# Performance work log

Hardware: AMD Instinct MI355X
Metric: run time of the kernel (lower is better)

## Reference

```python
import jax, jax.numpy as jnp
import numpy as np

N = 512          # number of ROI boxes
C = 1024         # detector box_head feature dim (in_feats)
HID_REPN = 256   # RePN hidden
HID = 256        # GAT hidden per head
HEADS = 4
NUM_CLASSES = 91
IMG_H, IMG_W = 800.0, 800.0
NEG_SLOPE = 0.2  # PyG GATConv default leaky relu slope


def setup_inputs() -> dict:
    key = jax.random.key(0)
    ks = jax.random.split(key, 12)
    s = 0.05
    feats = jax.random.normal(ks[0], (N, C), jnp.float32)
    # valid boxes: x1<x2, y1<y2, inside 800x800 image
    xy = jax.random.uniform(ks[1], (N, 2), jnp.float32, 0.0, 600.0)
    wh = jax.random.uniform(ks[2], (N, 2), jnp.float32, 10.0, 200.0)
    boxes = jnp.concatenate([xy, xy + wh], axis=1)
    # RelationProposalNetwork params (fc1: [hid, 2C+4], fc2: [1, hid])
    repn_w1 = jax.random.normal(ks[3], (HID_REPN, 2 * C + 4), jnp.float32) * s
    repn_b1 = jnp.zeros((HID_REPN,), jnp.float32)
    repn_w2 = jax.random.normal(ks[4], (1, HID_REPN), jnp.float32) * s
    repn_b2 = jnp.zeros((1,), jnp.float32)
    # AttentionalGCN: GATConv1 (in=C+4 -> HID, HEADS, concat), GATConv2 (HEADS*HID -> NUM_CLASSES, 1 head)
    gat1_w = jax.random.normal(ks[5], (C + 4, HEADS * HID), jnp.float32) * s
    gat1_asrc = jax.random.normal(ks[6], (HEADS, HID), jnp.float32) * s
    gat1_adst = jax.random.normal(ks[7], (HEADS, HID), jnp.float32) * s
    gat1_b = jnp.zeros((HEADS * HID,), jnp.float32)
    gat2_w = jax.random.normal(ks[8], (HEADS * HID, NUM_CLASSES), jnp.float32) * s
    gat2_asrc = jax.random.normal(ks[9], (1, NUM_CLASSES), jnp.float32) * s
    gat2_adst = jax.random.normal(ks[10], (1, NUM_CLASSES), jnp.float32) * s
    gat2_b = jnp.zeros((NUM_CLASSES,), jnp.float32)
    return dict(feats=feats, boxes=boxes,
                repn_w1=repn_w1, repn_b1=repn_b1, repn_w2=repn_w2, repn_b2=repn_b2,
                gat1_w=gat1_w, gat1_asrc=gat1_asrc, gat1_adst=gat1_adst, gat1_b=gat1_b,
                gat2_w=gat2_w, gat2_asrc=gat2_asrc, gat2_adst=gat2_adst, gat2_b=gat2_b,
                k=5)


def _gat_conv(x, src, dst, W, a_src, a_dst, bias, n, heads, out_c, concat_heads):
    # PyG GATConv: h = xW, e_uv = leakyrelu(a_src.h_u + a_dst.h_v), softmax over incoming
    # edges of target v, out_v = sum_u alpha_uv h_u (+ bias). Self-loops already in src/dst.
    h = (x @ W).reshape(n, heads, out_c)                       # [N,H,F]
    a_s = jnp.einsum('nhf,hf->nh', h, a_src)                   # [N,H]
    a_d = jnp.einsum('nhf,hf->nh', h, a_dst)
    e = jax.nn.leaky_relu(a_s[src] + a_d[dst], NEG_SLOPE)      # [E,H]
    m = jax.ops.segment_max(e, dst, num_segments=n)            # [N,H]
    m = jnp.where(jnp.isfinite(m), m, 0.0)
    ex = jnp.exp(e - m[dst])
    denom = jax.ops.segment_sum(ex, dst, num_segments=n)
    alpha = ex / (denom[dst] + 1e-16)                          # [E,H]
    out = jax.ops.segment_sum(alpha[:, :, None] * h[src], dst, num_segments=n)  # [N,H,F]
    out = out.reshape(n, heads * out_c) if concat_heads else out.mean(axis=1)
    return out + bias


def reference(feats, boxes, repn_w1, repn_b1, repn_w2, repn_b2,
              gat1_w, gat1_asrc, gat1_adst, gat1_b,
              gat2_w, gat2_asrc, gat2_adst, gat2_b, k):
    n, c = feats.shape
    # --- RelationProposalNetwork: fc1(cat[f_i, f_j, |b_i-b_j|]) without materializing [N,N,2C+4]
    wf1, wf2, wg = repn_w1[:, :c], repn_w1[:, c:2 * c], repn_w1[:, 2 * c:]
    p1 = feats @ wf1.T                                          # [N,hid]
    p2 = feats @ wf2.T                                          # [N,hid]
    geom_pair = jnp.abs(boxes[:, None, :] - boxes[None, :, :])  # [N,N,4]
    pg = jnp.einsum('ijd,hd->ijh', geom_pair, wg)               # [N,N,hid]
    h = jax.nn.relu(p1[:, None, :] + p2[None, :, :] + pg + repn_b1)
    rel = jnp.einsum('ijh,h->ij', h, repn_w2[0]) + repn_b2[0]   # [N,N] relation scores
    # --- kNN graph via topk (skip self at rank 0), as in _make_edge_index (N > k branch)
    _, idx = jax.lax.top_k(rel, k + 1)
    nbrs = idx[:, 1:]                                           # [N,k]
    src = jnp.repeat(jnp.arange(n), k)
    dst = nbrs.reshape(-1)
    loop = jnp.arange(n)                                        # PyG GATConv adds self-loops
    src = jnp.concatenate([src, loop])
    dst = jnp.concatenate([dst, loop])
    # --- node features: [roi_feats, normalized box geometry]
    scale = jnp.array([IMG_W, IMG_H, IMG_W, IMG_H], jnp.float32)
    nb = boxes / scale
    geom = jnp.stack([nb[:, 0], nb[:, 1], nb[:, 2] - nb[:, 0], nb[:, 3] - nb[:, 1]], axis=1)
    x = jnp.concatenate([feats, geom], axis=1)                  # [N, C+4]
    # --- AttentionalGCN: relu(GAT1) -> GAT2
    h1 = jax.nn.relu(_gat_conv(x, src, dst, gat1_w, gat1_asrc, gat1_adst, gat1_b, n, HEADS, HID, True))
    logits = _gat_conv(h1, src, dst, gat2_w, gat2_asrc, gat2_adst, gat2_b, n, 1, NUM_CLASSES, True)
    probs = jax.nn.softmax(logits, axis=1)                      # per-node class probs
    return logits, probs, rel
```

## Files before the change

kernel.cpp:

```cpp
#include <hip/hip_runtime.h>

#define NCLS 91
#define W1_LD 2052

typedef __attribute__((ext_vector_type(8))) short short8;
typedef __attribute__((ext_vector_type(4))) float f32x4;

__device__ inline ushort bf16_rne(float x) {
    unsigned u = __float_as_uint(x);
    return (ushort)((u + 0x7fffu + ((u >> 16) & 1u)) >> 16);
}

__global__ __launch_bounds__(128) void k_pre(const float* __restrict__ feats,
                                             const float* __restrict__ Wg,
                                             ushort* __restrict__ Afh,
                                             ushort* __restrict__ Afl,
                                             ushort* __restrict__ Bfh,
                                             ushort* __restrict__ Bfl,
                                             int* __restrict__ zero_ints,
                                             const float* __restrict__ w1f,
                                             float* __restrict__ pp) {
    int b = blockIdx.x, tid = threadIdx.x;
    __shared__ float As[64 * 32];
    __shared__ float Bs[64 * 64];
    if (b < 1536) {
        if (b < 4) zero_ints[b * 128 + tid] = 0;
        int lane = tid & 63;
        float x[8];
        size_t off;
        ushort *oh, *ol;
        if (b < 512) {
            int g = b * 128 + tid;
            int q = g >> 6;
            int it = q & 31, kt = q >> 5;
            int row = it * 16 + (lane & 15);
            int col0 = kt * 32 + (lane >> 4) * 8;
            const float* src = feats + row * 1024 + col0;
            float4 u0 = *(const float4*)(src);
            float4 u1 = *(const float4*)(src + 4);
            x[0] = u0.x; x[1] = u0.y; x[2] = u0.z; x[3] = u0.w;
            x[4] = u1.x; x[5] = u1.y; x[6] = u1.z; x[7] = u1.w;
            off = ((size_t)(kt * 32 + it) * 64 + lane) * 8;
            oh = Afh; ol = Afl;
        } else {
            int g = (b - 512) * 128 + tid;
            int q = g >> 6;
            int nt = q & 63, kt = q >> 6;
            int col = nt * 16 + (lane & 15);
            int row0 = kt * 32 + (lane >> 4) * 8;
#pragma unroll
            for (int e = 0; e < 8; ++e) x[e] = Wg[(row0 + e) * 1024 + col];
            off = ((size_t)(kt * 64 + nt) * 64 + lane) * 8;
            oh = Bfh; ol = Bfl;
        }
        uint uh[4], ul[4];
#pragma unroll
        for (int p = 0; p < 4; ++p) {
            ushort h0 = bf16_rne(x[2 * p]);
            ushort h1 = bf16_rne(x[2 * p + 1]);
            float f0 = __uint_as_float((unsigned)h0 << 16);
            float f1 = __uint_as_float((unsigned)h1 << 16);
            ushort l0 = bf16_rne(x[2 * p] - f0);
            ushort l1 = bf16_rne(x[2 * p + 1] - f1);
            uh[p] = (uint)h0 | ((uint)h1 << 16);
            ul[p] = (uint)l0 | ((uint)l1 << 16);
        }
        *(uint4*)(oh + off) = make_uint4(uh[0], uh[1], uh[2], uh[3]);
        *(uint4*)(ol + off) = make_uint4(ul[0], ul[1], ul[2], ul[3]);
        return;
    }
    int bx = b - 1536;
    int r0 = (bx & 7) * 64, i0 = ((bx >> 3) & 15) * 32, z = bx >> 7;
    int tx = tid & 15, ty = tid >> 4;
    float* pout = pp + z * 262144;
    int ai = tid & 31, akq = (tid >> 5) * 16;
    int br = tid & 63, bkq = (tid >> 6) * 32;
    const float* abase = feats + (i0 + ai) * 1024 + z * 128 + akq;
    int rg = r0 + br;
    const float* bbase = w1f + (rg < 256 ? rg * W1_LD : (rg - 256) * W1_LD + 1024)
                       + z * 128 + bkq;
    float4 av[4], bv[8];
#pragma unroll
    for (int s = 0; s < 4; ++s) av[s] = *(const float4*)(abase + 4 * s);
#pragma unroll
    for (int s = 0; s < 8; ++s) bv[s] = *(const float4*)(bbase + 4 * s);
    float acc[4][4] = {};
    for (int kt = 0; kt < 2; ++kt) {
#pragma unroll
        for (int s = 0; s < 4; ++s) {
            int k = akq + 4 * s;
            As[(k + 0) * 32 + ai] = av[s].x; As[(k + 1) * 32 + ai] = av[s].y;
            As[(k + 2) * 32 + ai] = av[s].z; As[(k + 3) * 32 + ai] = av[s].w;
        }
#pragma unroll
        for (int s = 0; s < 8; ++s) {
            int k = bkq + 4 * s;
            Bs[(k + 0) * 64 + br] = bv[s].x; Bs[(k + 1) * 64 + br] = bv[s].y;
            Bs[(k + 2) * 64 + br] = bv[s].z; Bs[(k + 3) * 64 + br] = bv[s].w;
        }
        __syncthreads();
        if (kt + 1 < 2) {
#pragma unroll
            for (int s = 0; s < 4; ++s) av[s] = *(const float4*)(abase + 64 + 4 * s);
#pragma unroll
            for (int s = 0; s < 8; ++s) bv[s] = *(const float4*)(bbase + 64 + 4 * s);
        }
#pragma unroll
        for (int k = 0; k < 64; ++k) {
            float4 a4 = *(const float4*)(As + k * 32 + ty * 4);
            float4 b4 = *(const float4*)(Bs + k * 64 + tx * 4);
            acc[0][0] = fmaf(a4.x, b4.x, acc[0][0]); acc[0][1] = fmaf(a4.x, b4.y, acc[0][1]);
            acc[0][2] = fmaf(a4.x, b4.z, acc[0][2]); acc[0][3] = fmaf(a4.x, b4.w, acc[0][3]);
            acc[1][0] = fmaf(a4.y, b4.x, acc[1][0]); acc[1][1] = fmaf(a4.y, b4.y, acc[1][1]);
            acc[1][2] = fmaf(a4.y, b4.z, acc[1][2]); acc[1][3] = fmaf(a4.y, b4.w, acc[1][3]);
            acc[2][0] = fmaf(a4.z, b4.x, acc[2][0]); acc[2][1] = fmaf(a4.z, b4.y, acc[2][1]);
            acc[2][2] = fmaf(a4.z, b4.z, acc[2][2]); acc[2][3] = fmaf(a4.z, b4.w, acc[2][3]);
            acc[3][0] = fmaf(a4.w, b4.x, acc[3][0]); acc[3][1] = fmaf(a4.w, b4.y, acc[3][1]);
            acc[3][2] = fmaf(a4.w, b4.z, acc[3][2]); acc[3][3] = fmaf(a4.w, b4.w, acc[3][3]);
        }
        __syncthreads();
    }
#pragma unroll
    for (int ii = 0; ii < 4; ++ii)
        *(float4*)(pout + (i0 + ty * 4 + ii) * 512 + r0 + tx * 4) =
            make_float4(acc[ii][0], acc[ii][1], acc[ii][2], acc[ii][3]);
}

__global__ __launch_bounds__(256) void k_psum(const float* __restrict__ pp,
                                              float* __restrict__ ppsum) {
    int idx = (blockIdx.x * 256 + threadIdx.x) * 4;
    float4 a = *(const float4*)(pp + idx);
#pragma unroll
    for (int p = 1; p < 8; ++p) {
        float4 v = *(const float4*)(pp + p * 262144 + idx);
        a.x += v.x; a.y += v.y; a.z += v.z; a.w += v.w;
    }
    *(float4*)(ppsum + idx) = a;
}

__global__ __launch_bounds__(256) void k_relmm(const float* __restrict__ ppsum,
                                               const float* __restrict__ w1f,
                                               const float* __restrict__ b1f,
                                               const float* __restrict__ w2f,
                                               const float* __restrict__ boxesf,
                                               float* __restrict__ r0,
                                               float* __restrict__ prel,
                                               const ushort* __restrict__ Afh,
                                               const ushort* __restrict__ Afl,
                                               const ushort* __restrict__ Bfh,
                                               const ushort* __restrict__ Bfl,
                                               float* __restrict__ P) {
    __shared__ union SM {
        struct { float As1[32 * 17]; float Bs[32 * 64]; float Awg[32 * 4]; float Aw2[32]; } r;
        uint4 buf[2][4][4][64];
    } sm;
    int b = blockIdx.x;
    if (b < 1024) {
        int j0 = (b & 7) * 64, i0 = ((b >> 3) & 31) * 16, z = b >> 8;
        int tid = threadIdx.x, tx = tid & 63, ty = tid >> 6;
        float* As1 = sm.r.As1;
        float* Bs  = sm.r.Bs;
        float* Awg = sm.r.Awg;
        float* Aw2 = sm.r.Aw2;
        float4 bj = *(const float4*)(boxesf + (j0 + tx) * 4);
        float g[4][4];
#pragma unroll
        for (int s = 0; s < 4; ++s) {
            float4 bi = *(const float4*)(boxesf + (i0 + ty * 4 + s) * 4);
            g[s][0] = fabsf(bi.x - bj.x); g[s][1] = fabsf(bi.y - bj.y);
            g[s][2] = fabsf(bi.z - bj.z); g[s][3] = fabsf(bi.w - bj.w);
        }
        float acc[4] = {0.f, 0.f, 0.f, 0.f};
        int ali = tid & 15, alh = (tid >> 4) * 4;
        int blj = tid & 63, blh = (tid >> 6) * 8;
        for (int c4 = 0; c4 < 2; ++c4) {
            int hb = (z * 2 + c4) * 32;
            if (tid < 128) {
                float4 a4 = *(const float4*)(ppsum + (i0 + ali) * 512 + hb + alh);
                float4 bb = *(const float4*)(b1f + hb + alh);
                As1[(alh + 0) * 17 + ali] = a4.x + bb.x;
                As1[(alh + 1) * 17 + ali] = a4.y + bb.y;
                As1[(alh + 2) * 17 + ali] = a4.z + bb.z;
                As1[(alh + 3) * 17 + ali] = a4.w + bb.w;
            }
#pragma unroll
            for (int s = 0; s < 2; ++s) {
                int h = blh + 4 * s;
                float4 u4 = *(const float4*)(ppsum + (j0 + blj) * 512 + 256 + hb + h);
                Bs[(h + 0) * 64 + blj] = u4.x;
                Bs[(h + 1) * 64 + blj] = u4.y;
                Bs[(h + 2) * 64 + blj] = u4.z;
                Bs[(h + 3) * 64 + blj] = u4.w;
            }
            if (tid < 32) {
                int hg = hb + tid;
                *(float4*)(Awg + tid * 4) = *(const float4*)(w1f + hg * W1_LD + 2048);
                Aw2[tid] = w2f[hg];
            }
            __syncthreads();
#pragma unroll
            for (int hh = 0; hh < 32; ++hh) {
                float4 wg = *(const float4*)(Awg + hh * 4);
                float w2v = Aw2[hh];
                float p2v = Bs[hh * 64 + tx];
                float s0 = As1[hh * 17 + ty * 4 + 0];
                float s1 = As1[hh * 17 + ty * 4 + 1];
                float s2 = As1[hh * 17 + ty * 4 + 2];
                float s3 = As1[hh * 17 + ty * 4 + 3];
                float t0 = s0 + p2v;
                t0 = fmaf(g[0][0], wg.x, t0); t0 = fmaf(g[0][1], wg.y, t0);
                t0 = fmaf(g[0][2], wg.z, t0); t0 = fmaf(g[0][3], wg.w, t0);
                acc[0] = fmaf(w2v, fmaxf(t0, 0.f), acc[0]);
                float t1 = s1 + p2v;
                t1 = fmaf(g[1][0], wg.x, t1); t1 = fmaf(g[1][1], wg.y, t1);
                t1 = fmaf(g[1][2], wg.z, t1); t1 = fmaf(g[1][3], wg.w, t1);
                acc[1] = fmaf(w2v, fmaxf(t1, 0.f), acc[1]);
                float t2 = s2 + p2v;
                t2 = fmaf(g[2][0], wg.x, t2); t2 = fmaf(g[2][1], wg.y, t2);
                t2 = fmaf(g[2][2], wg.z, t2); t2 = fmaf(g[2][3], wg.w, t2);
                acc[2] = fmaf(w2v, fmaxf(t2, 0.f), acc[2]);
                float t3 = s3 + p2v;
                t3 = fmaf(g[3][0], wg.x, t3); t3 = fmaf(g[3][1], wg.y, t3);
                t3 = fmaf(g[3][2], wg.z, t3); t3 = fmaf(g[3][3], wg.w, t3);
                acc[3] = fmaf(w2v, fmaxf(t3, 0.f), acc[3]);
            }
            __syncthreads();
        }
        float* po = (z == 0) ? r0 : (prel + (z - 1) * 262144);
#pragma unroll
        for (int s = 0; s < 4; ++s)
            po[(i0 + ty * 4 + s) * 512 + j0 + tx] = acc[s];
        return;
    }
    int m = b - 1024;
    int nt0 = (m & 15) * 4, it0 = ((m >> 4) & 7) * 4, z = m >> 7;
    int t = threadIdx.x, lane = t & 63, w = t >> 6;
    int wr = w >> 1, wc = w & 1, sub = w;
    const uint4* gAh = (const uint4*)Afh;
    const uint4* gAl = (const uint4*)Afl;
    const uint4* gBh = (const uint4*)Bfh;
    const uint4* gBl = (const uint4*)Bfl;
    f32x4 acc[2][2];
    f32x4 zero = {0.f, 0.f, 0.f, 0.f};
    acc[0][0] = zero; acc[0][1] = zero; acc[1][0] = zero; acc[1][1] = zero;
    int ktg = z * 8;
    uint4 rah = gAh[(ktg * 32 + it0 + sub) * 64 + lane];
    uint4 ral = gAl[(ktg * 32 + it0 + sub) * 64 + lane];
    uint4 rbh = gBh[(ktg * 64 + nt0 + sub) * 64 + lane];
    uint4 rbl = gBl[(ktg * 64 + nt0 + sub) * 64 + lane];
    for (int kk = 0; kk < 8; ++kk) {
        int cur = kk & 1;
        sm.buf[cur][0][sub][lane] = rah;
        sm.buf[cur][1][sub][lane] = ral;
        sm.buf[cur][2][sub][lane] = rbh;
        sm.buf[cur][3][sub][lane] = rbl;
        __syncthreads();
        if (kk < 7) {
            int kn = ktg + kk + 1;
            rah = gAh[(kn * 32 + it0 + sub) * 64 + lane];
            ral = gAl[(kn * 32 + it0 + sub) * 64 + lane];
            rbh = gBh[(kn * 64 + nt0 + sub) * 64 + lane];
            rbl = gBl[(kn * 64 + nt0 + sub) * 64 + lane];
        }
        short8 ah[2], al[2], bh[2], bl[2];
#pragma unroll
        for (int i = 0; i < 2; ++i) {
            ah[i] = *(const short8*)&sm.buf[cur][0][2 * wr + i][lane];
            al[i] = *(const short8*)&sm.buf[cur][1][2 * wr + i][lane];
            bh[i] = *(const short8*)&sm.buf[cur][2][2 * wc + i][lane];
            bl[i] = *(const short8*)&sm.buf[cur][3][2 * wc + i][lane];
        }
#pragma unroll
        for (int i = 0; i < 2; ++i)
#pragma unroll
            for (int j = 0; j < 2; ++j) {
                acc[i][j] = __builtin_amdgcn_mfma_f32_16x16x32_bf16(ah[i], bh[j], acc[i][j], 0, 0, 0);
                acc[i][j] = __builtin_amdgcn_mfma_f32_16x16x32_bf16(ah[i], bl[j], acc[i][j], 0, 0, 0);
                acc[i][j] = __builtin_amdgcn_mfma_f32_16x16x32_bf16(al[i], bh[j], acc[i][j], 0, 0, 0);
            }
        __syncthreads();
    }
    float* outp = P + z * 524288;
#pragma unroll
    for (int i = 0; i < 2; ++i)
#pragma unroll
        for (int j = 0; j < 2; ++j) {
            int rbase = (it0 + 2 * wr + i) * 16 + (lane >> 4) * 4;
            int c = (nt0 + 2 * wc + j) * 16 + (lane & 15);
#pragma unroll
            for (int r = 0; r < 4; ++r)
                outp[(size_t)(rbase + r) * 1024 + c] = acc[i][j][r];
        }
}

__global__ __launch_bounds__(256) void k_tkep(const float* __restrict__ P,
                                              const float* __restrict__ boxesf,
                                              const float* __restrict__ Wg,
                                              const float* __restrict__ asrcf,
                                              const float* __restrict__ adstf,
                                              float* __restrict__ hX,
                                              float* __restrict__ a_s1,
                                              float* __restrict__ a_d1,
                                              const float* __restrict__ r0,
                                              const float* __restrict__ prel,
                                              const float* __restrict__ b2f,
                                              const int* __restrict__ kp,
                                              int* __restrict__ nbrs,
                                              int* __restrict__ count,
                                              float* __restrict__ rel_out) {
    __shared__ float rs[4][4], rd[4][4];
    int t = threadIdx.x;
    if (blockIdx.x >= 512) {
        if (t >= 64) return;
        int i = blockIdx.x - 512, lane = t;
        int k = *kp;
        float b2v = b2f[0];
        float v[8]; int ids[8];
        for (int q = 0; q < 8; ++q) {
            int j = lane + 64 * q;
            float val = r0[i * 512 + j] + prel[i * 512 + j]
                      + prel[262144 + i * 512 + j] + prel[524288 + i * 512 + j] + b2v;
            rel_out[i * 512 + j] = val;
            v[q] = val;
            ids[q] = j;
        }
        for (int pick = 0; pick < k + 1; ++pick) {
            float bv = -INFINITY; int bidx = 1 << 30;
            for (int q = 0; q < 8; ++q)
                if (v[q] > bv || (v[q] == bv && ids[q] < bidx)) { bv = v[q]; bidx = ids[q]; }
            for (int off = 32; off > 0; off >>= 1) {
                float ov = __shfl_down(bv, off);
                int oi = __shfl_down(bidx, off);
                if (ov > bv || (ov == bv && oi < bidx)) { bv = ov; bidx = oi; }
            }
            bv = __shfl(bv, 0); bidx = __shfl(bidx, 0);
            if (pick >= 1 && lane == 0) {
                nbrs[i * 8 + (pick - 1)] = bidx;
                atomicAdd(&count[bidx], 1);
            }
            for (int q = 0; q < 8; ++q) if (ids[q] == bidx) v[q] = -INFINITY;
        }
        if (lane == 0) atomicAdd(&count[i], 1);
        return;
    }
    int i = blockIdx.x;
    const float* P0 = P;
    const float* P1 = P + 524288;
    const float* P2 = P + 1048576;
    const float* P3 = P + 1572864;
    float4 bx = *(const float4*)(boxesf + i * 4);
    float g0 = bx.x / 800.f, g1 = bx.y / 800.f;
    float g2 = bx.z / 800.f - g0, g3 = bx.w / 800.f - g1;
    float ps[4], pd[4];
#pragma unroll
    for (int q = 0; q < 4; ++q) {
        int c = q * 256 + t;
        float v = P0[i * 1024 + c] + P1[i * 1024 + c] + P2[i * 1024 + c] + P3[i * 1024 + c];
        v = fmaf(g0, Wg[1024 * 1024 + c], v);
        v = fmaf(g1, Wg[1025 * 1024 + c], v);
        v = fmaf(g2, Wg[1026 * 1024 + c], v);
        v = fmaf(g3, Wg[1027 * 1024 + c], v);
        hX[i * 1024 + c] = v;
        ps[q] = v * asrcf[c];
        pd[q] = v * adstf[c];
    }
    int wid = t >> 6;
#pragma unroll
    for (int off = 32; off > 0; off >>= 1) {
#pragma unroll
        for (int q = 0; q < 4; ++q) {
            ps[q] += __shfl_down(ps[q], off);
            pd[q] += __shfl_down(pd[q], off);
        }
    }
    if ((t & 63) == 0) {
#pragma unroll
        for (int q = 0; q < 4; ++q) { rs[wid][q] = ps[q]; rd[wid][q] = pd[q]; }
    }
    __syncthreads();
    if (t < 4)
        a_s1[i * 4 + t] = rs[0][t] + rs[1][t] + rs[2][t] + rs[3][t];
    else if (t < 8) {
        int q = t - 4;
        a_d1[i * 4 + q] = rd[0][q] + rd[1][q] + rd[2][q] + rd[3][q];
    }
}

__global__ void k_scanfill(const int* __restrict__ count, const int* __restrict__ nbrs,
                           const int* __restrict__ kp,
                           int* __restrict__ offs, int* __restrict__ inlist) {
    __shared__ int s[512];
    __shared__ int excl[512];
    __shared__ int cur[512];
    int t = threadIdx.x;
    int c = count[t];
    s[t] = c; cur[t] = 0;
    __syncthreads();
    for (int off = 1; off < 512; off <<= 1) {
        int v = (t >= off) ? s[t - off] : 0;
        __syncthreads();
        s[t] += v;
        __syncthreads();
    }
    offs[t + 1] = s[t];
    if (t == 0) offs[0] = 0;
    excl[t] = s[t] - c;
    __syncthreads();
    int k = *kp;
    for (int q = 0; q < k; ++q) {
        int d = nbrs[t * 8 + q] & 511;
        int pos = atomicAdd(&cur[d], 1);
        inlist[excl[d] + pos] = t;
    }
    int pos = atomicAdd(&cur[t], 1);
    inlist[excl[t] + pos] = t;
}

__global__ __launch_bounds__(256) void k_ag12(const float* __restrict__ hX,
                                              const float* __restrict__ a_s,
                                              const float* __restrict__ a_d,
                                              const int* __restrict__ offs,
                                              const int* __restrict__ inlist,
                                              const float* __restrict__ bias1,
                                              const float* __restrict__ Wf,
                                              const float* __restrict__ asrcf,
                                              const float* __restrict__ adstf,
                                              float* __restrict__ h2,
                                              float* __restrict__ a_s2,
                                              float* __restrict__ a_d2) {
    int n = blockIdx.x, t = threadIdx.x;
    int beg = offs[n], deg = offs[n + 1] - beg;
    if (deg > 513) deg = 513;
    __shared__ int srcs[520];
    __shared__ float alpha[520][4];
    __shared__ float sm[4];
    __shared__ float xs[1024];
    __shared__ float hbuf[NCLS];
    __shared__ float sred[256], dred[256];
    for (int e = t; e < deg; e += 256) srcs[e] = inlist[beg + e] & 511;
    __syncthreads();
    for (int idx = t; idx < deg * 4; idx += 256) {
        int e = idx >> 2, q = idx & 3;
        float sc = a_s[srcs[e] * 4 + q] + a_d[n * 4 + q];
        alpha[e][q] = (sc >= 0.f) ? sc : 0.2f * sc;
    }
    __syncthreads();
    if (t < 4) {
        float m = -INFINITY;
        for (int e = 0; e < deg; ++e) m = fmaxf(m, alpha[e][t]);
        if (!isfinite(m)) m = 0.f;
        float s = 0.f;
        for (int e = 0; e < deg; ++e) { float ex = expf(alpha[e][t] - m); alpha[e][t] = ex; s += ex; }
        sm[t] = s + 1e-16f;
    }
    __syncthreads();
    for (int idx = t; idx < deg * 4; idx += 256) {
        int e = idx >> 2, q = idx & 3;
        alpha[e][q] /= sm[q];
    }
    __syncthreads();
    for (int q = 0; q < 4; ++q) {
        float acc = 0.f;
        for (int e = 0; e < deg; ++e) acc += alpha[e][q] * hX[srcs[e] * 1024 + q * 256 + t];
        xs[q * 256 + t] = fmaxf(acc + bias1[q * 256 + t], 0.f);
    }
    __syncthreads();
    int cls = t & 127, kh = t >> 7;
    float acc = 0.f;
    if (cls < NCLS) {
        const float* wp = Wf + (kh * 512) * NCLS + cls;
        const float* xp = xs + kh * 512;
        float a0 = 0.f, a1 = 0.f, a2 = 0.f, a3 = 0.f;
        for (int c = 0; c < 512; c += 4) {
            a0 = fmaf(xp[c + 0], wp[(c + 0) * NCLS], a0);
            a1 = fmaf(xp[c + 1], wp[(c + 1) * NCLS], a1);
            a2 = fmaf(xp[c + 2], wp[(c + 2) * NCLS], a2);
            a3 = fmaf(xp[c + 3], wp[(c + 3) * NCLS], a3);
        }
        acc = (a0 + a1) + (a2 + a3);
    }
    if (kh == 0 && cls < NCLS) hbuf[cls] = acc;
    __syncthreads();
    float tot = 0.f;
    int act = (kh == 1 && cls < NCLS);
    if (act) { tot = acc + hbuf[cls]; h2[n * NCLS + cls] = tot; }
    sred[t] = act ? tot * asrcf[cls] : 0.f;
    dred[t] = act ? tot * adstf[cls] : 0.f;
    __syncthreads();
    for (int s = 128; s > 0; s >>= 1) {
        if (t < s) { sred[t] += sred[t + s]; dred[t] += dred[t + s]; }
        __syncthreads();
    }
    if (t == 0) { a_s2[n] = sred[0]; a_d2[n] = dred[0]; }
}

__global__ void k_aggr2(const float* __restrict__ h2,
                        const float* __restrict__ a_s2, const float* __restrict__ a_d2,
                        const int* __restrict__ offs, const int* __restrict__ inlist,
                        const float* __restrict__ bias,
                        float* __restrict__ logits_out,
                        float* __restrict__ probs_out) {
    int n = blockIdx.x, t = threadIdx.x;
    int beg = offs[n], deg = offs[n + 1] - beg;
    if (deg > 513) deg = 513;
    __shared__ int srcs[520];
    __shared__ float alpha[520];
    __shared__ float red[128];
    __shared__ float smden;
    for (int e = t; e < deg; e += 128) {
        int s = inlist[beg + e] & 511;
        srcs[e] = s;
        float sc = a_s2[s] + a_d2[n];
        alpha[e] = (sc >= 0.f) ? sc : 0.2f * sc;
    }
    __syncthreads();
    if (t == 0) {
        float m = -INFINITY;
        for (int e = 0; e < deg; ++e) m = fmaxf(m, alpha[e]);
        if (!isfinite(m)) m = 0.f;
        float s = 0.f;
        for (int e = 0; e < deg; ++e) { float ex = expf(alpha[e] - m); alpha[e] = ex; s += ex; }
        smden = s + 1e-16f;
    }
    __syncthreads();
    float logit = 0.f;
    if (t < NCLS) {
        float acc = 0.f;
        for (int e = 0; e < deg; ++e) acc += alpha[e] * h2[srcs[e] * NCLS + t];
        logit = acc / smden + bias[t];
        logits_out[n * NCLS + t] = logit;
    }
    red[t] = (t < NCLS) ? logit : -INFINITY; __syncthreads();
    for (int s = 64; s > 0; s >>= 1) { if (t < s) red[t] = fmaxf(red[t], red[t + s]); __syncthreads(); }
    float mx = red[0];
    __syncthreads();
    float ex = (t < NCLS) ? expf(logit - mx) : 0.f;
    red[t] = ex; __syncthreads();
    for (int s = 64; s > 0; s >>= 1) { if (t < s) red[t] += red[t + s]; __syncthreads(); }
    float inv = 1.f / red[0];
    if (t < NCLS) probs_out[n * NCLS + t] = ex * inv;
}

extern "C" void kernel_launch(void* const* d_in, const int* in_sizes, int n_in,
                              void* d_out, int out_size, void* d_ws, size_t ws_size,
                              hipStream_t stream) {
    const float* feats   = (const float*)d_in[0];
    const float* boxes   = (const float*)d_in[1];
    const float* repn_w1 = (const float*)d_in[2];
    const float* repn_b1 = (const float*)d_in[3];
    const float* repn_w2 = (const float*)d_in[4];
    const float* repn_b2 = (const float*)d_in[5];
    const float* gat1_w    = (const float*)d_in[6];
    const float* gat1_asrc = (const float*)d_in[7];
    const float* gat1_adst = (const float*)d_in[8];
    const float* gat1_b    = (const float*)d_in[9];
    const float* gat2_w    = (const float*)d_in[10];
    const float* gat2_asrc = (const float*)d_in[11];
    const float* gat2_adst = (const float*)d_in[12];
    const float* gat2_b    = (const float*)d_in[13];
    const int* kp = (const int*)d_in[14];

    float* out = (float*)d_out;
    float* logits_out = out;
    float* probs_out  = out + 512 * NCLS;
    float* rel_out    = out + 2 * 512 * NCLS;

    float* wsf   = (float*)d_ws;
    float* pp    = wsf;
    float* P     = wsf;
    float* hX    = P;
    float* ppsum = wsf + 2097152;
    float* prel  = wsf + 2359296;
    ushort* Afh  = (ushort*)(wsf + 3145728);
    ushort* Afl  = (ushort*)(wsf + 3407872);
    ushort* Bfh  = (ushort*)(wsf + 3670016);
    ushort* Bfl  = (ushort*)(wsf + 4194304);
    float* h2    = wsf + 4718592;
    float* a_s2  = wsf + 4765696;
    float* a_d2  = wsf + 4766208;
    float* a_s1  = wsf + 4766720;
    float* a_d1  = wsf + 4768768;
    int* ib      = (int*)(wsf + 4770816);
    int* count   = ib;
    int* nbrs    = ib + 1024;
    int* offs    = ib + 5120;
    int* inlist  = ib + 5640;

    k_pre<<<dim3(2560), dim3(128), 0, stream>>>(feats, gat1_w, Afh, Afl, Bfh, Bfl,
                                                ib, repn_w1, pp);
    k_psum<<<dim3(256), dim3(256), 0, stream>>>(pp, ppsum);
    k_relmm<<<dim3(1536), dim3(256), 0, stream>>>(ppsum, repn_w1, repn_b1, repn_w2,
                                                  boxes, rel_out, prel,
                                                  Afh, Afl, Bfh, Bfl, P);
    k_tkep<<<dim3(1024), dim3(256), 0, stream>>>(P, boxes, gat1_w, gat1_asrc, gat1_adst,
                                                 hX, a_s1, a_d1,
                                                 rel_out, prel, repn_b2, kp,
                                                 nbrs, count, rel_out);
    k_scanfill<<<dim3(1), dim3(512), 0, stream>>>(count, nbrs, kp, offs, inlist);
    k_ag12<<<dim3(512), dim3(256), 0, stream>>>(hX, a_s1, a_d1, offs, inlist, gat1_b,
                                                gat2_w, gat2_asrc, gat2_adst,
                                                h2, a_s2, a_d2);
    k_aggr2<<<dim3(512), dim3(128), 0, stream>>>(h2, a_s2, a_d2, offs, inlist, gat2_b,
                                                 logits_out, probs_out);
}
```

Measured before the change: 172.4 us.

## Drop CSR scan kernel; each aggregation block scans neighbor list for incoming edges

Removes the single-block prefix-scan/fill kernel and the count atomics and zeroing. Each aggregation block now scans the full kNN neighbor table to find the sources pointing to its node and builds its incoming list in shared memory with shared atomics. This removes a serial single-block launch and global atomics, at the cost of every block reading the whole 512x8 neighbor array twice (once per GAT layer). Edge order within a node may change, which can perturb floating-point summation order.

```diff
diff --git a/kernel.cpp b/kernel.cpp
--- a/kernel.cpp
+++ b/kernel.cpp
@@ -17,14 +17,12 @@
                                              ushort* __restrict__ Afl,
                                              ushort* __restrict__ Bfh,
                                              ushort* __restrict__ Bfl,
-                                             int* __restrict__ zero_ints,
                                              const float* __restrict__ w1f,
                                              float* __restrict__ pp) {
     int b = blockIdx.x, tid = threadIdx.x;
     __shared__ float As[64 * 32];
     __shared__ float Bs[64 * 64];
     if (b < 1536) {
-        if (b < 4) zero_ints[b * 128 + tid] = 0;
         int lane = tid & 63;
         float x[8];
         size_t off;
@@ -306,7 +304,6 @@
                                               const float* __restrict__ b2f,
                                               const int* __restrict__ kp,
                                               int* __restrict__ nbrs,
-                                              int* __restrict__ count,
                                               float* __restrict__ rel_out) {
     __shared__ float rs[4][4], rd[4][4];
     int t = threadIdx.x;
@@ -334,13 +331,9 @@
                 if (ov > bv || (ov == bv && oi < bidx)) { bv = ov; bidx = oi; }
             }
             bv = __shfl(bv, 0); bidx = __shfl(bidx, 0);
-            if (pick >= 1 && lane == 0) {
-                nbrs[i * 8 + (pick - 1)] = bidx;
-                atomicAdd(&count[bidx], 1);
-            }
+            if (pick >= 1 && lane == 0) nbrs[i * 8 + (pick - 1)] = bidx;
             for (int q = 0; q < 8; ++q) if (ids[q] == bidx) v[q] = -INFINITY;
         }
-        if (lane == 0) atomicAdd(&count[i], 1);
         return;
     }
     int i = blockIdx.x;
@@ -386,41 +379,11 @@
     }
 }
 
-__global__ void k_scanfill(const int* __restrict__ count, const int* __restrict__ nbrs,
-                           const int* __restrict__ kp,
-                           int* __restrict__ offs, int* __restrict__ inlist) {
-    __shared__ int s[512];
-    __shared__ int excl[512];
-    __shared__ int cur[512];
-    int t = threadIdx.x;
-    int c = count[t];
-    s[t] = c; cur[t] = 0;
-    __syncthreads();
-    for (int off = 1; off < 512; off <<= 1) {
-        int v = (t >= off) ? s[t - off] : 0;
-        __syncthreads();
-        s[t] += v;
-        __syncthreads();
-    }
-    offs[t + 1] = s[t];
-    if (t == 0) offs[0] = 0;
-    excl[t] = s[t] - c;
-    __syncthreads();
-    int k = *kp;
-    for (int q = 0; q < k; ++q) {
-        int d = nbrs[t * 8 + q] & 511;
-        int pos = atomicAdd(&cur[d], 1);
-        inlist[excl[d] + pos] = t;
-    }
-    int pos = atomicAdd(&cur[t], 1);
-    inlist[excl[t] + pos] = t;
-}
-
 __global__ __launch_bounds__(256) void k_ag12(const float* __restrict__ hX,
                                               const float* __restrict__ a_s,
                                               const float* __restrict__ a_d,
-                                              const int* __restrict__ offs,
-                                              const int* __restrict__ inlist,
+                                              const int* __restrict__ nbrs,
+                                              const int* __restrict__ kp,
                                               const float* __restrict__ bias1,
                                               const float* __restrict__ Wf,
                                               const float* __restrict__ asrcf,
@@ -429,16 +392,27 @@
                                               float* __restrict__ a_s2,
                                               float* __restrict__ a_d2) {
     int n = blockIdx.x, t = threadIdx.x;
-    int beg = offs[n], deg = offs[n + 1] - beg;
-    if (deg > 513) deg = 513;
+    __shared__ int cnt;
     __shared__ int srcs[520];
     __shared__ float alpha[520][4];
-    __shared__ float sm[4];
+    __shared__ float smx[4];
     __shared__ float xs[1024];
     __shared__ float hbuf[NCLS];
     __shared__ float sred[256], dred[256];
-    for (int e = t; e < deg; e += 256) srcs[e] = inlist[beg + e] & 511;
-    __syncthreads();
+    if (t == 0) { cnt = 0; srcs[0] = n; }
+    __syncthreads();
+    int k = *kp; if (k > 8) k = 8;
+#pragma unroll
+    for (int r = 0; r < 2; ++r) {
+        int i = t * 2 + r;
+        for (int q = 0; q < k; ++q)
+            if ((nbrs[i * 8 + q] & 511) == n) {
+                int p = atomicAdd(&cnt, 1);
+                srcs[p + 1] = i;
+            }
+    }
+    __syncthreads();
+    int deg = cnt + 1; if (deg > 513) deg = 513;
     for (int idx = t; idx < deg * 4; idx += 256) {
         int e = idx >> 2, q = idx & 3;
         float sc = a_s[srcs[e] * 4 + q] + a_d[n * 4 + q];
@@ -451,12 +425,12 @@
         if (!isfinite(m)) m = 0.f;
         float s = 0.f;
         for (int e = 0; e < deg; ++e) { float ex = expf(alpha[e][t] - m); alpha[e][t] = ex; s += ex; }
-        sm[t] = s + 1e-16f;
+        smx[t] = s + 1e-16f;
     }
     __syncthreads();
     for (int idx = t; idx < deg * 4; idx += 256) {
         int e = idx >> 2, q = idx & 3;
-        alpha[e][q] /= sm[q];
+        alpha[e][q] /= smx[q];
     }
     __syncthreads();
     for (int q = 0; q < 4; ++q) {
@@ -494,22 +468,36 @@
     if (t == 0) { a_s2[n] = sred[0]; a_d2[n] = dred[0]; }
 }
 
-__global__ void k_aggr2(const float* __restrict__ h2,
-                        const float* __restrict__ a_s2, const float* __restrict__ a_d2,
-                        const int* __restrict__ offs, const int* __restrict__ inlist,
-                        const float* __restrict__ bias,
-                        float* __restrict__ logits_out,
-                        float* __restrict__ probs_out) {
+__global__ __launch_bounds__(128) void k_aggr2(const float* __restrict__ h2,
+                                               const float* __restrict__ a_s2,
+                                               const float* __restrict__ a_d2,
+                                               const int* __restrict__ nbrs,
+                                               const int* __restrict__ kp,
+                                               const float* __restrict__ bias,
+                                               float* __restrict__ logits_out,
+                                               float* __restrict__ probs_out) {
     int n = blockIdx.x, t = threadIdx.x;
-    int beg = offs[n], deg = offs[n + 1] - beg;
-    if (deg > 513) deg = 513;
+    __shared__ int cnt;
     __shared__ int srcs[520];
     __shared__ float alpha[520];
     __shared__ float red[128];
     __shared__ float smden;
+    if (t == 0) { cnt = 0; srcs[0] = n; }
+    __syncthreads();
+    int k = *kp; if (k > 8) k = 8;
+#pragma unroll
+    for (int r = 0; r < 4; ++r) {
+        int i = t * 4 + r;
+        for (int q = 0; q < k; ++q)
+            if ((nbrs[i * 8 + q] & 511) == n) {
+                int p = atomicAdd(&cnt, 1);
+                srcs[p + 1] = i;
+            }
+    }
+    __syncthreads();
+    int deg = cnt + 1; if (deg > 513) deg = 513;
     for (int e = t; e < deg; e += 128) {
-        int s = inlist[beg + e] & 511;
-        srcs[e] = s;
+        int s = srcs[e];
         float sc = a_s2[s] + a_d2[n];
         alpha[e] = (sc >= 0.f) ? sc : 0.2f * sc;
     }
@@ -580,14 +568,10 @@
     float* a_d2  = wsf + 4766208;
     float* a_s1  = wsf + 4766720;
     float* a_d1  = wsf + 4768768;
-    int* ib      = (int*)(wsf + 4770816);
-    int* count   = ib;
-    int* nbrs    = ib + 1024;
-    int* offs    = ib + 5120;
-    int* inlist  = ib + 5640;
+    int* nbrs    = (int*)(wsf + 4770816) + 1024;
 
     k_pre<<<dim3(2560), dim3(128), 0, stream>>>(feats, gat1_w, Afh, Afl, Bfh, Bfl,
-                                                ib, repn_w1, pp);
+                                                repn_w1, pp);
     k_psum<<<dim3(256), dim3(256), 0, stream>>>(pp, ppsum);
     k_relmm<<<dim3(1536), dim3(256), 0, stream>>>(ppsum, repn_w1, repn_b1, repn_w2,
                                                   boxes, rel_out, prel,
@@ -595,11 +579,10 @@
     k_tkep<<<dim3(1024), dim3(256), 0, stream>>>(P, boxes, gat1_w, gat1_asrc, gat1_adst,
                                                  hX, a_s1, a_d1,
                                                  rel_out, prel, repn_b2, kp,
-                                                 nbrs, count, rel_out);
-    k_scanfill<<<dim3(1), dim3(512), 0, stream>>>(count, nbrs, kp, offs, inlist);
-    k_ag12<<<dim3(512), dim3(256), 0, stream>>>(hX, a_s1, a_d1, offs, inlist, gat1_b,
+                                                 nbrs, rel_out);
+    k_ag12<<<dim3(512), dim3(256), 0, stream>>>(hX, a_s1, a_d1, nbrs, kp, gat1_b,
                                                 gat2_w, gat2_asrc, gat2_adst,
                                                 h2, a_s2, a_d2);
-    k_aggr2<<<dim3(512), dim3(128), 0, stream>>>(h2, a_s2, a_d2, offs, inlist, gat2_b,
+    k_aggr2<<<dim3(512), dim3(128), 0, stream>>>(h2, a_s2, a_d2, nbrs, kp, gat2_b,
                                                  logits_out, probs_out);
 }
```

Result: no change. 173.9 us, median of 2 (+0.9%).
